# Kernel optimization log

Measured on AMD Instinct MI355X. Metric: run time of the kernel, lower is better.

The kernel has to match this reference:

```python
import jax, jax.numpy as jnp
import numpy as np

K = 256       # num states
M = 2         # markov order
D = 256       # lemb_size
V = 50000     # ntypes (vocab)
T = 512
B = 256
Kp1 = K + 1
EPS = 1e-5
INIT = 0.1


def _layernorm(h, g, b):
    mu = h.mean(-1, keepdims=True)
    var = ((h - mu) ** 2).mean(-1, keepdims=True)
    return (h - mu) / jnp.sqrt(var + EPS) * g + b


def setup_inputs() -> dict:
    key = jax.random.key(0)
    ks = jax.random.split(key, 12)
    u = lambda k, shp: jax.random.uniform(k, shp, jnp.float32, -INIT, INIT)
    return {
        "x": jax.random.randint(ks[0], (T, B), 0, V, dtype=jnp.int32),
        "z": jax.random.randint(ks[1], (T, B), 0, K, dtype=jnp.int32),
        "lembs": u(ks[2], (K, D)),
        "tlembs": u(ks[3], (Kp1, D)),
        "dec_W": u(ks[4], (V, D)),
        "dec_b": jnp.zeros((V,), jnp.float32),
        "em_W": u(ks[5], (D, D)),
        "em_bias": jnp.zeros((D,), jnp.float32),
        "em_g": jnp.ones((D,), jnp.float32),
        "em_beta": jnp.zeros((D,), jnp.float32),
        "td_W": u(ks[6], (K, M * D)),
        "td_b": jnp.zeros((K,), jnp.float32),
        "tm_W": u(ks[7], (M * D, M * D)),
        "tm_bias": jnp.zeros((M * D,), jnp.float32),
        "tn_g": jnp.ones((M * D,), jnp.float32),
        "tn_beta": jnp.zeros((M * D,), jnp.float32),
    }


def reference(x, z, lembs, tlembs, dec_W, dec_b, em_W, em_bias, em_g, em_beta,
              td_W, td_b, tm_W, tm_bias, tn_g, tn_beta):
    # --- emission distribution: K x V log-normalized ---
    h = _layernorm(lembs + jax.nn.relu(lembs @ em_W.T + em_bias), em_g, em_beta)
    emdist = jax.nn.log_softmax(h @ dec_W.T + dec_b, axis=1)  # (K, V)

    # --- transition distribution: (Kp1^M, K) log-normalized ---
    # cartesian product of label embeddings, row-major: row r <-> (i_0,...,i_{M-1})
    idx = jnp.indices((Kp1,) * M).reshape(M, -1)                 # (M, Kp1^M)
    cat = tlembs[idx].transpose(1, 0, 2).reshape(-1, M * D)      # (Kp1^M, M*D)
    th = _layernorm(cat + jax.nn.relu(cat @ tm_W.T + tm_bias), tn_g, tn_beta)
    transdist = jax.nn.log_softmax(th @ td_W.T + td_b, axis=1)   # (Kp1^M, K)

    # --- log_joint ---
    xlps = emdist.T[x]                                           # (T, B, K)
    emlps = jnp.take_along_axis(xlps, z[..., None].astype(jnp.int32), axis=2)[..., 0].sum(0)  # (B,)

    zpad = jnp.concatenate([jnp.full((M, B), K, dtype=z.dtype), z], axis=0)  # (T+M, B)
    win = jnp.stack([zpad[m:m + T] for m in range(M + 1)], 0)    # (M+1, T, B)
    lin = win[0]
    for m in range(1, M):
        lin = lin * Kp1 + win[m]                                 # row index into (Kp1^M, K)
    trans_lps = transdist[lin, win[M]]                           # (T, B)
    return emlps + trans_lps.sum(0)                              # (B,)
```

## Files before the change

### kernel.cpp

```cpp
#include <hip/hip_runtime.h>

#define Kst 256
#define Dd 256
#define Vv 50000
#define VPAD 50176
#define Tt 512
#define Bb 256
#define KP1 257
#define MD 512
#define NROWS (KP1*KP1)
#define EPSf 1e-5f

#define VB2 196
#define NP1 (VB2*4)
#define NTR ((NROWS+31)/32)
#define EMB 800

typedef __attribute__((ext_vector_type(8))) short short8;
typedef __attribute__((ext_vector_type(4))) float f32x4;
typedef __attribute__((ext_vector_type(4))) unsigned u32x4;
typedef __attribute__((ext_vector_type(2))) unsigned u32x2;

__device__ __forceinline__ unsigned short f2bf(float f) {
    unsigned u = __builtin_bit_cast(unsigned, f);
    unsigned r = (u + 0x7fffu + ((u >> 16) & 1u)) >> 16;
    return (unsigned short)r;
}
__device__ __forceinline__ float bf2f(unsigned short u) {
    return __builtin_bit_cast(float, ((unsigned)u) << 16);
}
__device__ __forceinline__ unsigned bfpack(float lo, float hi) {
    return __builtin_amdgcn_perm(__builtin_bit_cast(unsigned, hi),
                                 __builtin_bit_cast(unsigned, lo), 0x07060302u);
}
__device__ __forceinline__ unsigned f2bf2(float lo, float hi) {
    return (unsigned)f2bf(lo) | ((unsigned)f2bf(hi) << 16);
}

union HPU {
    struct { short ta[32][264]; float lsep[4][32][2]; float musig[32][2]; } g;
    struct { short pl[64][266]; } p;
};

__global__ __launch_bounds__(256) void k_hP(
    const float* __restrict__ lembs, const float* __restrict__ em_W,
    const float* __restrict__ em_bias, const float* __restrict__ em_g,
    const float* __restrict__ em_beta, unsigned short* __restrict__ h_bf,
    const float* __restrict__ tlembs, const float* __restrict__ tm_W,
    float* __restrict__ P0, float* __restrict__ P1,
    const float* __restrict__ td_W, const float* __restrict__ tn_g,
    const float* __restrict__ tn_beta, const float* __restrict__ td_b,
    unsigned short* __restrict__ tdwg_bf, float* __restrict__ Gt,
    float* __restrict__ Bt, const float* __restrict__ dec_W,
    unsigned short* __restrict__ dwP)
{
    __shared__ HPU su;
    int bid = blockIdx.x;
    int tid = threadIdx.x, lane = tid & 63, wv = tid >> 6;
    int l15 = lane & 15, q = lane >> 4;

    if (bid >= 108) {
        int pb = bid - 108;
        int vb2 = pb >> 2, c = pb & 3;
        short (*pl)[266] = su.p.pl;
        int base_row = vb2*256 + c*64;
        #pragma unroll 4
        for (int i = 0; i < 16; ++i) {
            int row = wv*16 + i;
            int grow = base_row + row; if (grow > Vv-1) grow = Vv-1;
            float4 f = ((const float4*)(dec_W + (size_t)grow*Dd))[lane];
            u32x2 w; w.x = bfpack(f.x, f.y); w.y = bfpack(f.z, f.w);
            *(u32x2*)&pl[row][lane*4] = w;
        }
        __syncthreads();
        #pragma unroll
        for (int i = 0; i < 8; ++i) {
            short8 val = *(const short8*)&pl[(lane & 15)*4 + wv][i*32 + (lane >> 4)*8];
            *(short8*)(dwP + ((size_t)vb2*8192 + (size_t)i*1024
                              + (c*4 + wv)*64 + lane)*8) = val;
        }
        return;
    }

    if (bid >= 44) {
        int c = (bid - 44)*4 + wv;
        const float4* w4 = (const float4*)(td_W + (size_t)c*MD);
        const float4* g4 = (const float4*)tn_g;
        const float4* b4 = (const float4*)tn_beta;
        float sg = 0.f, sb = 0.f;
        short8 o;
        #pragma unroll
        for (int u = 0; u < 2; ++u) {
            int j4 = lane*2 + u;
            float4 w = w4[j4], g = g4[j4], bt = b4[j4];
            sg += w.x*g.x + w.y*g.y + w.z*g.z + w.w*g.w;
            sb += w.x*bt.x + w.y*bt.y + w.z*bt.z + w.w*bt.w;
            o[u*4+0] = (short)f2bf(w.x*g.x);
            o[u*4+1] = (short)f2bf(w.y*g.y);
            o[u*4+2] = (short)f2bf(w.z*g.z);
            o[u*4+3] = (short)f2bf(w.w*g.w);
        }
        {
            int wvv = c >> 6, l15v = (c >> 2) & 15, ctv = c & 3;
            int ksv = lane >> 2, qv = lane & 3;
            *(short8*)(tdwg_bf +
                ((((size_t)wvv*16 + ksv)*4 + ctv)*64 + (qv*16 + l15v))*8) = o;
        }
        #pragma unroll
        for (int dd = 32; dd > 0; dd >>= 1) {
            sg += __shfl_xor(sg, dd);
            sb += __shfl_xor(sb, dd);
        }
        if (lane == 0) { Gt[c] = sg; Bt[c] = sb + td_b[c]; }
        return;
    }

    short (*ta)[264] = su.g.ta;
    float (*lsep)[32][2] = su.g.lsep;
    float (*musig)[2] = su.g.musig;

    int job, r0, cb, koff, BK;
    const float* Arow; const float* Brow;
    if (bid < 8) {
        job = 0; r0 = bid*32; cb = 0; koff = 0; BK = Dd;
        Arow = lembs; Brow = em_W;
    } else {
        int b2 = bid - 8;
        int half = b2 / 18;
        int b3 = b2 % 18;
        job = 1 + half;
        r0 = (b3 >> 1) * 32;
        cb = (b3 & 1) * 256;
        koff = half * 256; BK = MD;
        Arow = tlembs; Brow = tm_W;
    }

    {
        int row = tid >> 3, seg = (tid & 7) * 32;
        int r = r0 + row;
        if (r > 256) r = 256;
        const float4* s4 = (const float4*)(Arow + (size_t)r*Dd + seg);
        #pragma unroll
        for (int u = 0; u < 4; ++u) {
            float4 f0 = s4[u*2], f1 = s4[u*2+1];
            u32x4 pk;
            pk.x = bfpack(f0.x, f0.y);
            pk.y = bfpack(f0.z, f0.w);
            pk.z = bfpack(f1.x, f1.y);
            pk.w = bfpack(f1.z, f1.w);
            *(short8*)&ta[row][seg + u*8] = __builtin_bit_cast(short8, pk);
        }
    }
    __syncthreads();

    const float* bptr[4];
    #pragma unroll
    for (int ct = 0; ct < 4; ++ct) {
        int j = cb + wv*64 + ct*16 + l15;
        bptr[ct] = Brow + (size_t)j*BK + koff + q*8;
    }
    f32x4 acc[2][4];
    #pragma unroll
    for (int rt = 0; rt < 2; ++rt)
        #pragma unroll
        for (int ct = 0; ct < 4; ++ct)
            acc[rt][ct] = (f32x4){0.f,0.f,0.f,0.f};
    for (int ks = 0; ks < 8; ++ks) {
        short8 a0 = *(const short8*)&ta[ 0 + l15][ks*32 + q*8];
        short8 a1 = *(const short8*)&ta[16 + l15][ks*32 + q*8];
        short8 b[4];
        #pragma unroll
        for (int ct = 0; ct < 4; ++ct) {
            float4 f0 = *(const float4*)(bptr[ct] + ks*32);
            float4 f1 = *(const float4*)(bptr[ct] + ks*32 + 4);
            u32x4 pk;
            pk.x = bfpack(f0.x, f0.y);
            pk.y = bfpack(f0.z, f0.w);
            pk.z = bfpack(f1.x, f1.y);
            pk.w = bfpack(f1.z, f1.w);
            b[ct] = __builtin_bit_cast(short8, pk);
        }
        #pragma unroll
        for (int ct = 0; ct < 4; ++ct) {
            acc[0][ct] = __builtin_amdgcn_mfma_f32_16x16x32_bf16(a0, b[ct], acc[0][ct], 0,0,0);
            acc[1][ct] = __builtin_amdgcn_mfma_f32_16x16x32_bf16(a1, b[ct], acc[1][ct], 0,0,0);
        }
    }

    if (job != 0) {
        float* Pd = (job == 1) ? P0 : P1;
        #pragma unroll
        for (int rt = 0; rt < 2; ++rt) {
            #pragma unroll
            for (int reg = 0; reg < 4; ++reg) {
                int r = r0 + rt*16 + q*4 + reg;
                if (r < KP1) {
                    float* dst = Pd + (size_t)r*MD + cb + wv*64;
                    #pragma unroll
                    for (int ct = 0; ct < 4; ++ct)
                        dst[ct*16 + l15] = acc[rt][ct][reg];
                }
            }
        }
        return;
    }

    float bias_c[4];
    #pragma unroll
    for (int ct = 0; ct < 4; ++ct)
        bias_c[ct] = em_bias[wv*64 + ct*16 + l15];
    #pragma unroll
    for (int rt = 0; rt < 2; ++rt) {
        #pragma unroll
        for (int reg = 0; reg < 4; ++reg) {
            int r = r0 + rt*16 + q*4 + reg;
            #pragma unroll
            for (int ct = 0; ct < 4; ++ct) {
                float lv = lembs[(size_t)r*Dd + wv*64 + ct*16 + l15];
                acc[rt][ct][reg] = lv + fmaxf(acc[rt][ct][reg] + bias_c[ct], 0.f);
            }
        }
    }
    #pragma unroll
    for (int rt = 0; rt < 2; ++rt) {
        #pragma unroll
        for (int reg = 0; reg < 4; ++reg) {
            float s  = ((acc[rt][0][reg] + acc[rt][1][reg]) + (acc[rt][2][reg] + acc[rt][3][reg]));
            float ss = ((acc[rt][0][reg]*acc[rt][0][reg] + acc[rt][1][reg]*acc[rt][1][reg])
                      + (acc[rt][2][reg]*acc[rt][2][reg] + acc[rt][3][reg]*acc[rt][3][reg]));
            s  += __shfl_xor(s, 1);  ss += __shfl_xor(ss, 1);
            s  += __shfl_xor(s, 2);  ss += __shfl_xor(ss, 2);
            s  += __shfl_xor(s, 4);  ss += __shfl_xor(ss, 4);
            s  += __shfl_xor(s, 8);  ss += __shfl_xor(ss, 8);
            if (l15 == 0) {
                int rw = rt*16 + q*4 + reg;
                lsep[wv][rw][0] = s;
                lsep[wv][rw][1] = ss;
            }
        }
    }
    __syncthreads();
    if (tid < 32) {
        float s  = (lsep[0][tid][0] + lsep[1][tid][0]) + (lsep[2][tid][0] + lsep[3][tid][0]);
        float ss = (lsep[0][tid][1] + lsep[1][tid][1]) + (lsep[2][tid][1] + lsep[3][tid][1]);
        float mu = s * (1.f/Dd);
        musig[tid][0] = mu;
        musig[tid][1] = rsqrtf(ss*(1.f/Dd) - mu*mu + EPSf);
    }
    __syncthreads();
    float gl[4], bl[4];
    #pragma unroll
    for (int ct = 0; ct < 4; ++ct) {
        gl[ct] = em_g[wv*64 + ct*16 + l15];
        bl[ct] = em_beta[wv*64 + ct*16 + l15];
    }
    #pragma unroll
    for (int rt = 0; rt < 2; ++rt) {
        #pragma unroll
        for (int reg = 0; reg < 4; ++reg) {
            int rw = rt*16 + q*4 + reg;
            int r = r0 + rw;
            float mu = musig[rw][0], rs = musig[rw][1];
            unsigned short* dst = h_bf + (size_t)r*Dd + wv*64;
            #pragma unroll
            for (int ct = 0; ct < 4; ++ct)
                dst[ct*16 + l15] = f2bf((acc[rt][ct][reg] - mu)*rs*gl[ct] + bl[ct]);
        }
    }
}

union SMemU {
    struct { short hs[64][264]; } em;
    struct { short th[32][520]; float musig[32][2]; float lsep[4][32][2]; } tr;
};

__global__ __launch_bounds__(256, 4) void k_emtrans(
    const unsigned short* __restrict__ dwP, const float* __restrict__ dec_b,
    const unsigned short* __restrict__ h_bf, float* __restrict__ part1,
    unsigned short* __restrict__ E2,
    const float* __restrict__ tlembs, const float* __restrict__ P0,
    const float* __restrict__ P1, const float* __restrict__ tm_bias,
    const short* __restrict__ tdwg_bf, const float* __restrict__ Gt,
    const float* __restrict__ Bt, float* __restrict__ lse_t,
    unsigned short* __restrict__ Td)
{
    __shared__ SMemU sm;
    int bid = blockIdx.x;
    int tid = threadIdx.x, lane = tid & 63, wv = tid >> 6;
    int l15 = lane & 15, q = lane >> 4;

    if (bid < EMB) {
        int xcd = bid & 7, slot = bid >> 3;
        int g2 = slot >> 2, kg = slot & 3;
        int vb = g2*8 + xcd;
        if (vb >= VB2) return;
        short (*hs)[264] = sm.em.hs;

        {
            int row = tid >> 2, c0 = (tid & 3) * 64;
            const short8* src = (const short8*)(h_bf + (size_t)(kg*64 + row)*Dd + c0);
            #pragma unroll
            for (int u = 0; u < 8; ++u)
                *(short8*)&hs[row][c0 + u*8] = src[u];
        }
        __syncthreads();

        f32x4 acc[4][4];
        #pragma unroll
        for (int mt = 0; mt < 4; ++mt)
            #pragma unroll
            for (int ct = 0; ct < 4; ++ct)
                acc[mt][ct] = (f32x4){0.f,0.f,0.f,0.f};

        const short8* bb8 = (const short8*)dwP + ((size_t)vb*8*16 + wv*4)*64 + lane;
        short8 Bf[3][4];
        #define LDB_EM(slot_, kk) { \
            Bf[slot_][0] = bb8[((kk)*16 + 0)*64]; \
            Bf[slot_][1] = bb8[((kk)*16 + 1)*64]; \
            Bf[slot_][2] = bb8[((kk)*16 + 2)*64]; \
            Bf[slot_][3] = bb8[((kk)*16 + 3)*64]; }
        LDB_EM(0, 0)
        LDB_EM(1, 1)
        #pragma unroll
        for (int ks = 0; ks < 8; ++ks) {
            if (ks < 6) LDB_EM((ks+2)%3, ks+2)
            short8 a[4];
            #pragma unroll
            for (int mt = 0; mt < 4; ++mt)
                a[mt] = *(const short8*)&hs[mt*16 + l15][ks*32 + q*8];
            #pragma unroll
            for (int mt = 0; mt < 4; ++mt)
                #pragma unroll
                for (int ct = 0; ct < 4; ++ct)
                    acc[mt][ct] = __builtin_amdgcn_mfma_f32_16x16x32_bf16(a[mt], Bf[ks%3][ct], acc[mt][ct], 0,0,0);
        }
        #undef LDB_EM

        int vcol[4]; bool vok[4];
        #pragma unroll
        for (int ct = 0; ct < 4; ++ct) {
            int v = vb*256 + wv*64 + l15*4 + ct;
            vok[ct] = (v < Vv);
            vcol[ct] = v < Vv ? v : Vv-1;
        }
        #pragma unroll
        for (int ct = 0; ct < 4; ++ct) {
            if (vok[ct]) {
                float db = dec_b[vcol[ct]];
                #pragma unroll
                for (int mt = 0; mt < 4; ++mt)
                    #pragma unroll
                    for (int reg = 0; reg < 4; ++reg)
                        acc[mt][ct][reg] += db;
            } else {
                #pragma unroll
                for (int mt = 0; mt < 4; ++mt)
                    #pragma unroll
                    for (int reg = 0; reg < 4; ++reg)
                        acc[mt][ct][reg] = -1e30f;
            }
        }
        #pragma unroll
        for (int mt = 0; mt < 4; ++mt) {
            #pragma unroll
            for (int reg = 0; reg < 4; ++reg) {
                int k = kg*64 + mt*16 + q*4 + reg;
                u32x2 p;
                p.x = f2bf2(acc[mt][0][reg], acc[mt][1][reg]);
                p.y = f2bf2(acc[mt][2][reg], acc[mt][3][reg]);
                *(u32x2*)(E2 + (size_t)k*VPAD + vb*256 + wv*64 + l15*4) = p;
            }
        }
        #pragma unroll
        for (int mt = 0; mt < 4; ++mt) {
            #pragma unroll
            for (int reg = 0; reg < 4; ++reg) {
                float s = (__expf(acc[mt][0][reg]) + __expf(acc[mt][1][reg]))
                        + (__expf(acc[mt][2][reg]) + __expf(acc[mt][3][reg]));
                s += __shfl_xor(s, 1);
                s += __shfl_xor(s, 2);
                s += __shfl_xor(s, 4);
                s += __shfl_xor(s, 8);
                if (l15 == 0) {
                    int k = kg*64 + mt*16 + q*4 + reg;
                    part1[(size_t)(vb*4 + wv)*256 + k] = s;
                }
            }
        }
        return;
    }

    int tr_id = bid - EMB;
    if (tr_id >= NTR) return;
    short (*th)[520]   = sm.tr.th;
    float (*musig)[2]  = sm.tr.musig;
    float (*lsep)[32][2] = sm.tr.lsep;
    int r0 = tr_id * 32;

    {
        const float4* bias0 = (const float4*)tm_bias;
        const float4* bias1 = (const float4*)(tm_bias + 256);
        float4 c0 = bias0[lane], c1 = bias1[lane];
        int i0a[8], i1a[8];
        #pragma unroll
        for (int i = 0; i < 8; ++i) {
            int r = r0 + wv*8 + i; if (r >= NROWS) r = NROWS - 1;
            i0a[i] = r / KP1; i1a[i] = r - i0a[i]*KP1;
        }
        #define ROWBODY(i, A0, B0, T0, A1, B1, T1) { \
            int row = wv*8 + (i); \
            float v0 = (T0).x + fmaxf((A0).x+(B0).x+c0.x, 0.f); \
            float v1 = (T0).y + fmaxf((A0).y+(B0).y+c0.y, 0.f); \
            float v2 = (T0).z + fmaxf((A0).z+(B0).z+c0.z, 0.f); \
            float v3 = (T0).w + fmaxf((A0).w+(B0).w+c0.w, 0.f); \
            float v4 = (T1).x + fmaxf((A1).x+(B1).x+c1.x, 0.f); \
            float v5 = (T1).y + fmaxf((A1).y+(B1).y+c1.y, 0.f); \
            float v6 = (T1).z + fmaxf((A1).z+(B1).z+c1.z, 0.f); \
            float v7 = (T1).w + fmaxf((A1).w+(B1).w+c1.w, 0.f); \
            u32x2 p0; p0.x = bfpack(v0, v1); p0.y = bfpack(v2, v3); \
            u32x2 p1; p1.x = bfpack(v4, v5); p1.y = bfpack(v6, v7); \
            *(u32x2*)&th[row][lane*4]       = p0; \
            *(u32x2*)&th[row][256 + lane*4] = p1; \
            float s  = ((v0+v1)+(v2+v3)) + ((v4+v5)+(v6+v7)); \
            float ss = ((v0*v0+v1*v1)+(v2*v2+v3*v3)) + ((v4*v4+v5*v5)+(v6*v6+v7*v7)); \
            _Pragma("unroll") \
            for (int d = 1; d < 64; d <<= 1) { \
                s  += __shfl_xor(s, d); \
                ss += __shfl_xor(ss, d); \
            } \
            if (lane == 0) { \
                float mu = s * (1.f/MD); \
                musig[row][0] = mu; \
                musig[row][1] = rsqrtf(ss*(1.f/MD) - mu*mu + EPSf); \
            } }

        if (i0a[0] == i0a[7]) {
            float4 A0 = ((const float4*)(P0 + (size_t)i0a[0]*MD))[lane];
            float4 A1 = ((const float4*)(P0 + (size_t)i0a[0]*MD + 256))[lane];
            float4 T0 = ((const float4*)(tlembs + (size_t)i0a[0]*Dd))[lane];
            float4 b0 = ((const float4*)(P1 + (size_t)i1a[0]*MD))[lane];
            float4 b1 = ((const float4*)(P1 + (size_t)i1a[0]*MD + 256))[lane];
            float4 t1 = ((const float4*)(tlembs + (size_t)i1a[0]*Dd))[lane];
            #pragma unroll
            for (int i = 0; i < 8; ++i) {
                float4 nb0, nb1, nt1;
                if (i < 7) {
                    nb0 = ((const float4*)(P1 + (size_t)i1a[i+1]*MD))[lane];
                    nb1 = ((const float4*)(P1 + (size_t)i1a[i+1]*MD + 256))[lane];
                    nt1 = ((const float4*)(tlembs + (size_t)i1a[i+1]*Dd))[lane];
                }
                ROWBODY(i, A0, b0, T0, A1, b1, t1)
                b0 = nb0; b1 = nb1; t1 = nt1;
            }
        } else {
            float4 A0 = ((const float4*)(P0 + (size_t)i0a[0]*MD))[lane];
            float4 A1 = ((const float4*)(P0 + (size_t)i0a[0]*MD + 256))[lane];
            float4 T0 = ((const float4*)(tlembs + (size_t)i0a[0]*Dd))[lane];
            float4 b0 = ((const float4*)(P1 + (size_t)i1a[0]*MD))[lane];
            float4 b1 = ((const float4*)(P1 + (size_t)i1a[0]*MD + 256))[lane];
            float4 t1 = ((const float4*)(tlembs + (size_t)i1a[0]*Dd))[lane];
            #pragma unroll
            for (int i = 0; i < 8; ++i) {
                float4 nA0, nA1, nT0, nb0, nb1, nt1;
                if (i < 7) {
                    nA0 = ((const float4*)(P0 + (size_t)i0a[i+1]*MD))[lane];
                    nA1 = ((const float4*)(P0 + (size_t)i0a[i+1]*MD + 256))[lane];
                    nT0 = ((const float4*)(tlembs + (size_t)i0a[i+1]*Dd))[lane];
                    nb0 = ((const float4*)(P1 + (size_t)i1a[i+1]*MD))[lane];
                    nb1 = ((const float4*)(P1 + (size_t)i1a[i+1]*MD + 256))[lane];
                    nt1 = ((const float4*)(tlembs + (size_t)i1a[i+1]*Dd))[lane];
                }
                ROWBODY(i, A0, b0, T0, A1, b1, t1)
                A0 = nA0; A1 = nA1; T0 = nT0; b0 = nb0; b1 = nb1; t1 = nt1;
            }
        }
        #undef ROWBODY
    }
    __syncthreads();

    f32x4 acc[2][4];
    #pragma unroll
    for (int rt = 0; rt < 2; ++rt)
        #pragma unroll
        for (int ct = 0; ct < 4; ++ct)
            acc[rt][ct] = (f32x4){0.f, 0.f, 0.f, 0.f};
    const short* bb = tdwg_bf + (size_t)wv*32768 + (size_t)lane*8;
    short8 Bf[3][4];
    #define LDB_TR(slot_, kk) { const short* nxt = bb + (size_t)(kk)*2048; \
        Bf[slot_][0] = *(const short8*)(nxt); \
        Bf[slot_][1] = *(const short8*)(nxt + 512); \
        Bf[slot_][2] = *(const short8*)(nxt + 1024); \
        Bf[slot_][3] = *(const short8*)(nxt + 1536); }
    LDB_TR(0, 0)
    LDB_TR(1, 1)
    #pragma unroll
    for (int ks = 0; ks < 16; ++ks) {
        if (ks < 14) LDB_TR((ks+2)%3, ks+2)
        int ko = ks*32 + q*8;
        short8 a0 = *(const short8*)&th[ 0 + l15][ko];
        short8 a1 = *(const short8*)&th[16 + l15][ko];
        acc[0][0] = __builtin_amdgcn_mfma_f32_16x16x32_bf16(a0, Bf[ks%3][0], acc[0][0], 0,0,0);
        acc[1][0] = __builtin_amdgcn_mfma_f32_16x16x32_bf16(a1, Bf[ks%3][0], acc[1][0], 0,0,0);
        acc[0][1] = __builtin_amdgcn_mfma_f32_16x16x32_bf16(a0, Bf[ks%3][1], acc[0][1], 0,0,0);
        acc[1][1] = __builtin_amdgcn_mfma_f32_16x16x32_bf16(a1, Bf[ks%3][1], acc[1][1], 0,0,0);
        acc[0][2] = __builtin_amdgcn_mfma_f32_16x16x32_bf16(a0, Bf[ks%3][2], acc[0][2], 0,0,0);
        acc[1][2] = __builtin_amdgcn_mfma_f32_16x16x32_bf16(a1, Bf[ks%3][2], acc[1][2], 0,0,0);
        acc[0][3] = __builtin_amdgcn_mfma_f32_16x16x32_bf16(a0, Bf[ks%3][3], acc[0][3], 0,0,0);
        acc[1][3] = __builtin_amdgcn_mfma_f32_16x16x32_bf16(a1, Bf[ks%3][3], acc[1][3], 0,0,0);
    }
    #undef LDB_TR

    float4 Gc = *(const float4*)(Gt + wv*64 + l15*4);
    float4 Bc = *(const float4*)(Bt + wv*64 + l15*4);
    #pragma unroll
    for (int rt = 0; rt < 2; ++rt) {
        #pragma unroll
        for (int reg = 0; reg < 4; ++reg) {
            int rw = rt*16 + q*4 + reg;
            float mu = musig[rw][0], rs = musig[rw][1];
            float e0 = rs*(acc[rt][0][reg] - mu*Gc.x) + Bc.x;
            float e1 = rs*(acc[rt][1][reg] - mu*Gc.y) + Bc.y;
            float e2 = rs*(acc[rt][2][reg] - mu*Gc.z) + Bc.z;
            float e3 = rs*(acc[rt][3][reg] - mu*Gc.w) + Bc.w;
            long r = (long)r0 + rw;
            if (r < NROWS) {
                u32x2 p;
                p.x = f2bf2(e0, e1);
                p.y = f2bf2(e2, e3);
                *(u32x2*)(Td + (size_t)r*Kst + wv*64 + l15*4) = p;
            }
            float m = fmaxf(fmaxf(e0, e1), fmaxf(e2, e3));
            m = fmaxf(m, __shfl_xor(m, 1));
            m = fmaxf(m, __shfl_xor(m, 2));
            m = fmaxf(m, __shfl_xor(m, 4));
            m = fmaxf(m, __shfl_xor(m, 8));
            float s = __expf(e0 - m) + __expf(e1 - m) + __expf(e2 - m) + __expf(e3 - m);
            s += __shfl_xor(s, 1);
            s += __shfl_xor(s, 2);
            s += __shfl_xor(s, 4);
            s += __shfl_xor(s, 8);
            if (l15 == 0) {
                lsep[wv][rw][0] = m;
                lsep[wv][rw][1] = s;
            }
        }
    }
    __syncthreads();
    if (tid < 32) {
        int r = r0 + tid;
        if (r < NROWS) {
            float m0 = lsep[0][tid][0], m1 = lsep[1][tid][0];
            float m2 = lsep[2][tid][0], m3 = lsep[3][tid][0];
            float mg = fmaxf(fmaxf(m0, m1), fmaxf(m2, m3));
            float s = lsep[0][tid][1]*__expf(m0-mg) + lsep[1][tid][1]*__expf(m1-mg)
                    + lsep[2][tid][1]*__expf(m2-mg) + lsep[3][tid][1]*__expf(m3-mg);
            lse_t[r] = mg + logf(s);
        }
    }
}

__global__ __launch_bounds__(256) void k_lse8(
    const float* __restrict__ part1, float* __restrict__ lpart)
{
    __shared__ float lemp[4][256];
    int tid = threadIdx.x, lane = tid & 63, w = tid >> 6;
    const f32x4* p4 = (const f32x4*)part1;
    f32x4 s4 = (f32x4){0.f,0.f,0.f,0.f};
    int j0 = blockIdx.x * 98;
    for (int j = j0 + w; j < j0 + 98; j += 4) {
        f32x4 v = p4[(size_t)j*64 + lane];
        s4.x += v.x; s4.y += v.y; s4.z += v.z; s4.w += v.w;
    }
    *(f32x4*)&lemp[w][lane*4] = s4;
    __syncthreads();
    lpart[blockIdx.x*256 + tid] = (lemp[0][tid] + lemp[1][tid]) + (lemp[2][tid] + lemp[3][tid]);
}

__global__ __launch_bounds__(256) void k_gather7(
    const int* __restrict__ x, const int* __restrict__ z,
    const unsigned short* __restrict__ E2, const float* __restrict__ lpart,
    const unsigned short* __restrict__ Td, const float* __restrict__ lse_t,
    float* __restrict__ gpart)
{
    __shared__ float lem[256];
    int tid = threadIdx.x;
    {
        float s = 0.f;
        #pragma unroll
        for (int r = 0; r < 8; ++r) s += lpart[r*256 + tid];
        lem[tid] = logf(s);
    }
    __syncthreads();

    int b = tid;
    int t0 = blockIdx.x * 8;
    int zm1 = (t0 >= 1) ? z[(t0-1)*Bb + b] : Kst;
    int zm2 = (t0 >= 2) ? z[(t0-2)*Bb + b] : Kst;
    float accv = 0.f;
    #pragma unroll
    for (int u = 0; u < 8; ++u) {
        int t = t0 + u;
        int zc = z[t*Bb + b];
        int xv = x[t*Bb + b];
        int lin = zm2*KP1 + zm1;
        accv += bf2f(E2[(size_t)zc*VPAD + xv]) - lem[zc]
              + bf2f(Td[(size_t)lin*Kst + zc]) - lse_t[lin];
        zm2 = zm1; zm1 = zc;
    }
    gpart[blockIdx.x*Bb + b] = accv;
}

__global__ __launch_bounds__(256) void k_fin(
    const float* __restrict__ gpart, float* __restrict__ out)
{
    int b = threadIdx.x;
    float s = 0.f;
    #pragma unroll 8
    for (int r = 0; r < 64; ++r)
        s += gpart[r*Bb + b];
    out[b] = s;
}

extern "C" void kernel_launch(void* const* d_in, const int* in_sizes, int n_in,
                              void* d_out, int out_size, void* d_ws, size_t ws_size,
                              hipStream_t stream)
{
    const int*   x       = (const int*)  d_in[0];
    const int*   z       = (const int*)  d_in[1];
    const float* lembs   = (const float*)d_in[2];
    const float* tlembs  = (const float*)d_in[3];
    const float* dec_W   = (const float*)d_in[4];
    const float* dec_b   = (const float*)d_in[5];
    const float* em_W    = (const float*)d_in[6];
    const float* em_bias = (const float*)d_in[7];
    const float* em_g    = (const float*)d_in[8];
    const float* em_beta = (const float*)d_in[9];
    const float* td_W    = (const float*)d_in[10];
    const float* td_b    = (const float*)d_in[11];
    const float* tm_W    = (const float*)d_in[12];
    const float* tm_bias = (const float*)d_in[13];
    const float* tn_g    = (const float*)d_in[14];
    const float* tn_beta = (const float*)d_in[15];
    float* out = (float*)d_out;

    float* ws     = (float*)d_ws;
    float* P0     = ws;
    float* P1     = P0 + 131584;
    float* part1  = P1 + 131584;
    float* lpart  = part1 + 200704;
    float* gpart  = lpart + 2048;
    float* lse_t  = gpart + 16384;
    float* Gt     = lse_t + 66052;
    float* Bt     = Gt + 256;
    unsigned short* tdwg_bf = (unsigned short*)(Bt + 256);
    unsigned short* h_bf   = tdwg_bf + 131072;
    unsigned short* E2     = h_bf + 65536;
    unsigned short* Td     = E2 + (size_t)Kst*VPAD;
    unsigned short* dwP    = Td + (size_t)NROWS*Kst;

    k_hP<<<108 + 784, 256, 0, stream>>>(lembs, em_W, em_bias, em_g, em_beta, h_bf,
                                        tlembs, tm_W, P0, P1,
                                        td_W, tn_g, tn_beta, td_b, tdwg_bf, Gt, Bt,
                                        dec_W, dwP);
    k_emtrans<<<EMB + NTR, 256, 0, stream>>>(
        dwP, dec_b, h_bf, part1, E2,
        tlembs, P0, P1, tm_bias, (const short*)tdwg_bf, Gt, Bt, lse_t, Td);
    k_lse8<<<8, 256, 0, stream>>>(part1, lpart);
    k_gather7<<<64, 256, 0, stream>>>(x, z, E2, lpart, Td, lse_t, gpart);
    k_fin<<<1, 256, 0, stream>>>(gpart, out);
}
```

Baseline: 203.6 us.

## Split weight packing into separate kernel and prepack em_W/tm_W into MFMA layout

Moves em_W and tm_W bf16 conversion into a new packing kernel that writes them in MFMA fragment order, so the small GEMM kernel loads ready-made bf16 fragments instead of converting fp32 on the fly. The epilogues now use a permuted column mapping so each lane writes float4/packed stores and reads vectorized bias, gamma and beta. The software-prefetch double buffering in the transition row loop is removed in favour of direct loads. The cost is an extra kernel launch with a serial dependency, and the row loop may lose latency hiding.

Result: slower. 210.9 us (+3.6%).

```diff
diff --git a/kernel.cpp b/kernel.cpp
--- a/kernel.cpp
+++ b/kernel.cpp
@@ -37,32 +37,21 @@
     return (unsigned)f2bf(lo) | ((unsigned)f2bf(hi) << 16);
 }
 
-union HPU {
-    struct { short ta[32][264]; float lsep[4][32][2]; float musig[32][2]; } g;
-    struct { short pl[64][266]; } p;
-};
-
-__global__ __launch_bounds__(256) void k_hP(
-    const float* __restrict__ lembs, const float* __restrict__ em_W,
-    const float* __restrict__ em_bias, const float* __restrict__ em_g,
-    const float* __restrict__ em_beta, unsigned short* __restrict__ h_bf,
-    const float* __restrict__ tlembs, const float* __restrict__ tm_W,
-    float* __restrict__ P0, float* __restrict__ P1,
+__global__ __launch_bounds__(256) void k_pack(
+    const float* __restrict__ dec_W, unsigned short* __restrict__ dwP,
+    const float* __restrict__ em_W, unsigned short* __restrict__ emWP,
+    const float* __restrict__ tm_W, unsigned short* __restrict__ tmWP,
     const float* __restrict__ td_W, const float* __restrict__ tn_g,
     const float* __restrict__ tn_beta, const float* __restrict__ td_b,
     unsigned short* __restrict__ tdwg_bf, float* __restrict__ Gt,
-    float* __restrict__ Bt, const float* __restrict__ dec_W,
-    unsigned short* __restrict__ dwP)
+    float* __restrict__ Bt)
 {
-    __shared__ HPU su;
+    __shared__ short pl[64][266];
     int bid = blockIdx.x;
     int tid = threadIdx.x, lane = tid & 63, wv = tid >> 6;
-    int l15 = lane & 15, q = lane >> 4;
-
-    if (bid >= 108) {
-        int pb = bid - 108;
-        int vb2 = pb >> 2, c = pb & 3;
-        short (*pl)[266] = su.p.pl;
+
+    if (bid < 784) {
+        int vb2 = bid >> 2, c = bid & 3;
         int base_row = vb2*256 + c*64;
         #pragma unroll 4
         for (int i = 0; i < 16; ++i) {
@@ -81,9 +70,46 @@
         }
         return;
     }
-
-    if (bid >= 44) {
-        int c = (bid - 44)*4 + wv;
+    if (bid < 788) {
+        int jc = bid - 784;
+        #pragma unroll 4
+        for (int i = 0; i < 16; ++i) {
+            int row = wv*16 + i;
+            int j = jc*64 + row;
+            float4 f = ((const float4*)(em_W + (size_t)j*Dd))[lane];
+            u32x2 w; w.x = bfpack(f.x, f.y); w.y = bfpack(f.z, f.w);
+            *(u32x2*)&pl[row][lane*4] = w;
+        }
+        __syncthreads();
+        #pragma unroll
+        for (int i = 0; i < 8; ++i) {
+            short8 val = *(const short8*)&pl[(lane & 15)*4 + wv][i*32 + (lane >> 4)*8];
+            *(short8*)(emWP + ((size_t)(i*16 + jc*4 + wv)*64 + lane)*8) = val;
+        }
+        return;
+    }
+    if (bid < 804) {
+        int idx = bid - 788;
+        int jb = idx >> 3, t = idx & 7, jc = t >> 1, kh = t & 1;
+        #pragma unroll 4
+        for (int i = 0; i < 16; ++i) {
+            int row = wv*16 + i;
+            int j = jb*256 + jc*64 + row;
+            float4 f = ((const float4*)(tm_W + (size_t)j*MD + kh*256))[lane];
+            u32x2 w; w.x = bfpack(f.x, f.y); w.y = bfpack(f.z, f.w);
+            *(u32x2*)&pl[row][lane*4] = w;
+        }
+        __syncthreads();
+        #pragma unroll
+        for (int i = 0; i < 8; ++i) {
+            int ksG = kh*8 + i;
+            short8 val = *(const short8*)&pl[(lane & 15)*4 + wv][i*32 + (lane >> 4)*8];
+            *(short8*)(tmWP + ((size_t)((jb*16 + ksG)*16 + jc*4 + wv)*64 + lane)*8) = val;
+        }
+        return;
+    }
+    {
+        int c = (bid - 804)*4 + wv;
         const float4* w4 = (const float4*)(td_W + (size_t)c*MD);
         const float4* g4 = (const float4*)tn_g;
         const float4* b4 = (const float4*)tn_beta;
@@ -112,18 +138,30 @@
             sb += __shfl_xor(sb, dd);
         }
         if (lane == 0) { Gt[c] = sg; Bt[c] = sb + td_b[c]; }
-        return;
-    }
-
-    short (*ta)[264] = su.g.ta;
-    float (*lsep)[32][2] = su.g.lsep;
-    float (*musig)[2] = su.g.musig;
-
-    int job, r0, cb, koff, BK;
-    const float* Arow; const float* Brow;
+    }
+}
+
+__global__ __launch_bounds__(256) void k_hP2(
+    const float* __restrict__ lembs, const float* __restrict__ em_bias,
+    const float* __restrict__ em_g, const float* __restrict__ em_beta,
+    unsigned short* __restrict__ h_bf, const float* __restrict__ tlembs,
+    float* __restrict__ P0, float* __restrict__ P1,
+    const unsigned short* __restrict__ emWP, const unsigned short* __restrict__ tmWP)
+{
+    __shared__ short ta[32][264];
+    __shared__ float lsep[4][32][2];
+    __shared__ float musig[32][2];
+    int bid = blockIdx.x;
+    int tid = threadIdx.x, lane = tid & 63, wv = tid >> 6;
+    int l15 = lane & 15, q = lane >> 4;
+
+    int job, r0, cb;
+    const float* Arow;
+    const short8* bb8;
     if (bid < 8) {
-        job = 0; r0 = bid*32; cb = 0; koff = 0; BK = Dd;
-        Arow = lembs; Brow = em_W;
+        job = 0; r0 = bid*32; cb = 0;
+        Arow = lembs;
+        bb8 = (const short8*)emWP + (size_t)(wv*4)*64 + lane;
     } else {
         int b2 = bid - 8;
         int half = b2 / 18;
@@ -131,8 +169,9 @@
         job = 1 + half;
         r0 = (b3 >> 1) * 32;
         cb = (b3 & 1) * 256;
-        koff = half * 256; BK = MD;
-        Arow = tlembs; Brow = tm_W;
+        int jb = cb >> 8;
+        Arow = tlembs;
+        bb8 = (const short8*)tmWP + ((size_t)(jb*16 + half*8)*16 + wv*4)*64 + lane;
     }
 
     {
@@ -153,38 +192,28 @@
     }
     __syncthreads();
 
-    const float* bptr[4];
-    #pragma unroll
-    for (int ct = 0; ct < 4; ++ct) {
-        int j = cb + wv*64 + ct*16 + l15;
-        bptr[ct] = Brow + (size_t)j*BK + koff + q*8;
-    }
     f32x4 acc[2][4];
     #pragma unroll
     for (int rt = 0; rt < 2; ++rt)
         #pragma unroll
         for (int ct = 0; ct < 4; ++ct)
             acc[rt][ct] = (f32x4){0.f,0.f,0.f,0.f};
+    #pragma unroll
     for (int ks = 0; ks < 8; ++ks) {
         short8 a0 = *(const short8*)&ta[ 0 + l15][ks*32 + q*8];
         short8 a1 = *(const short8*)&ta[16 + l15][ks*32 + q*8];
-        short8 b[4];
-        #pragma unroll
-        for (int ct = 0; ct < 4; ++ct) {
-            float4 f0 = *(const float4*)(bptr[ct] + ks*32);
-            float4 f1 = *(const float4*)(bptr[ct] + ks*32 + 4);
-            u32x4 pk;
-            pk.x = bfpack(f0.x, f0.y);
-            pk.y = bfpack(f0.z, f0.w);
-            pk.z = bfpack(f1.x, f1.y);
-            pk.w = bfpack(f1.z, f1.w);
-            b[ct] = __builtin_bit_cast(short8, pk);
-        }
-        #pragma unroll
-        for (int ct = 0; ct < 4; ++ct) {
-            acc[0][ct] = __builtin_amdgcn_mfma_f32_16x16x32_bf16(a0, b[ct], acc[0][ct], 0,0,0);
-            acc[1][ct] = __builtin_amdgcn_mfma_f32_16x16x32_bf16(a1, b[ct], acc[1][ct], 0,0,0);
-        }
+        short8 b0 = bb8[(ks*16 + 0)*64];
+        short8 b1 = bb8[(ks*16 + 1)*64];
+        short8 b2 = bb8[(ks*16 + 2)*64];
+        short8 b3 = bb8[(ks*16 + 3)*64];
+        acc[0][0] = __builtin_amdgcn_mfma_f32_16x16x32_bf16(a0, b0, acc[0][0], 0,0,0);
+        acc[1][0] = __builtin_amdgcn_mfma_f32_16x16x32_bf16(a1, b0, acc[1][0], 0,0,0);
+        acc[0][1] = __builtin_amdgcn_mfma_f32_16x16x32_bf16(a0, b1, acc[0][1], 0,0,0);
+        acc[1][1] = __builtin_amdgcn_mfma_f32_16x16x32_bf16(a1, b1, acc[1][1], 0,0,0);
+        acc[0][2] = __builtin_amdgcn_mfma_f32_16x16x32_bf16(a0, b2, acc[0][2], 0,0,0);
+        acc[1][2] = __builtin_amdgcn_mfma_f32_16x16x32_bf16(a1, b2, acc[1][2], 0,0,0);
+        acc[0][3] = __builtin_amdgcn_mfma_f32_16x16x32_bf16(a0, b3, acc[0][3], 0,0,0);
+        acc[1][3] = __builtin_amdgcn_mfma_f32_16x16x32_bf16(a1, b3, acc[1][3], 0,0,0);
     }
 
     if (job != 0) {
@@ -195,30 +224,27 @@
             for (int reg = 0; reg < 4; ++reg) {
                 int r = r0 + rt*16 + q*4 + reg;
                 if (r < KP1) {
-                    float* dst = Pd + (size_t)r*MD + cb + wv*64;
-                    #pragma unroll
-                    for (int ct = 0; ct < 4; ++ct)
-                        dst[ct*16 + l15] = acc[rt][ct][reg];
+                    float4 o;
+                    o.x = acc[rt][0][reg]; o.y = acc[rt][1][reg];
+                    o.z = acc[rt][2][reg]; o.w = acc[rt][3][reg];
+                    *(float4*)(Pd + (size_t)r*MD + cb + wv*64 + l15*4) = o;
                 }
             }
         }
         return;
     }
 
-    float bias_c[4];
-    #pragma unroll
-    for (int ct = 0; ct < 4; ++ct)
-        bias_c[ct] = em_bias[wv*64 + ct*16 + l15];
+    float4 bias4 = *(const float4*)(em_bias + wv*64 + l15*4);
     #pragma unroll
     for (int rt = 0; rt < 2; ++rt) {
         #pragma unroll
         for (int reg = 0; reg < 4; ++reg) {
             int r = r0 + rt*16 + q*4 + reg;
-            #pragma unroll
-            for (int ct = 0; ct < 4; ++ct) {
-                float lv = lembs[(size_t)r*Dd + wv*64 + ct*16 + l15];
-                acc[rt][ct][reg] = lv + fmaxf(acc[rt][ct][reg] + bias_c[ct], 0.f);
-            }
+            float4 lv = *(const float4*)(lembs + (size_t)r*Dd + wv*64 + l15*4);
+            acc[rt][0][reg] = lv.x + fmaxf(acc[rt][0][reg] + bias4.x, 0.f);
+            acc[rt][1][reg] = lv.y + fmaxf(acc[rt][1][reg] + bias4.y, 0.f);
+            acc[rt][2][reg] = lv.z + fmaxf(acc[rt][2][reg] + bias4.z, 0.f);
+            acc[rt][3][reg] = lv.w + fmaxf(acc[rt][3][reg] + bias4.w, 0.f);
         }
     }
     #pragma unroll
@@ -248,12 +274,8 @@
         musig[tid][1] = rsqrtf(ss*(1.f/Dd) - mu*mu + EPSf);
     }
     __syncthreads();
-    float gl[4], bl[4];
-    #pragma unroll
-    for (int ct = 0; ct < 4; ++ct) {
-        gl[ct] = em_g[wv*64 + ct*16 + l15];
-        bl[ct] = em_beta[wv*64 + ct*16 + l15];
-    }
+    float4 g4  = *(const float4*)(em_g + wv*64 + l15*4);
+    float4 be4 = *(const float4*)(em_beta + wv*64 + l15*4);
     #pragma unroll
     for (int rt = 0; rt < 2; ++rt) {
         #pragma unroll
@@ -261,10 +283,14 @@
             int rw = rt*16 + q*4 + reg;
             int r = r0 + rw;
             float mu = musig[rw][0], rs = musig[rw][1];
-            unsigned short* dst = h_bf + (size_t)r*Dd + wv*64;
-            #pragma unroll
-            for (int ct = 0; ct < 4; ++ct)
-                dst[ct*16 + l15] = f2bf((acc[rt][ct][reg] - mu)*rs*gl[ct] + bl[ct]);
+            float e0 = (acc[rt][0][reg] - mu)*rs*g4.x + be4.x;
+            float e1 = (acc[rt][1][reg] - mu)*rs*g4.y + be4.y;
+            float e2 = (acc[rt][2][reg] - mu)*rs*g4.z + be4.z;
+            float e3 = (acc[rt][3][reg] - mu)*rs*g4.w + be4.w;
+            u32x2 p;
+            p.x = f2bf2(e0, e1);
+            p.y = f2bf2(e2, e3);
+            *(u32x2*)(h_bf + (size_t)r*Dd + wv*64 + l15*4) = p;
         }
     }
 }
@@ -438,40 +464,23 @@
             float4 A0 = ((const float4*)(P0 + (size_t)i0a[0]*MD))[lane];
             float4 A1 = ((const float4*)(P0 + (size_t)i0a[0]*MD + 256))[lane];
             float4 T0 = ((const float4*)(tlembs + (size_t)i0a[0]*Dd))[lane];
-            float4 b0 = ((const float4*)(P1 + (size_t)i1a[0]*MD))[lane];
-            float4 b1 = ((const float4*)(P1 + (size_t)i1a[0]*MD + 256))[lane];
-            float4 t1 = ((const float4*)(tlembs + (size_t)i1a[0]*Dd))[lane];
             #pragma unroll
             for (int i = 0; i < 8; ++i) {
-                float4 nb0, nb1, nt1;
-                if (i < 7) {
-                    nb0 = ((const float4*)(P1 + (size_t)i1a[i+1]*MD))[lane];
-                    nb1 = ((const float4*)(P1 + (size_t)i1a[i+1]*MD + 256))[lane];
-                    nt1 = ((const float4*)(tlembs + (size_t)i1a[i+1]*Dd))[lane];
-                }
+                float4 b0 = ((const float4*)(P1 + (size_t)i1a[i]*MD))[lane];
+                float4 b1 = ((const float4*)(P1 + (size_t)i1a[i]*MD + 256))[lane];
+                float4 t1 = ((const float4*)(tlembs + (size_t)i1a[i]*Dd))[lane];
                 ROWBODY(i, A0, b0, T0, A1, b1, t1)
-                b0 = nb0; b1 = nb1; t1 = nt1;
             }
         } else {
-            float4 A0 = ((const float4*)(P0 + (size_t)i0a[0]*MD))[lane];
-            float4 A1 = ((const float4*)(P0 + (size_t)i0a[0]*MD + 256))[lane];
-            float4 T0 = ((const float4*)(tlembs + (size_t)i0a[0]*Dd))[lane];
-            float4 b0 = ((const float4*)(P1 + (size_t)i1a[0]*MD))[lane];
-            float4 b1 = ((const float4*)(P1 + (size_t)i1a[0]*MD + 256))[lane];
-            float4 t1 = ((const float4*)(tlembs + (size_t)i1a[0]*Dd))[lane];
             #pragma unroll
             for (int i = 0; i < 8; ++i) {
-                float4 nA0, nA1, nT0, nb0, nb1, nt1;
-                if (i < 7) {
-                    nA0 = ((const float4*)(P0 + (size_t)i0a[i+1]*MD))[lane];
-                    nA1 = ((const float4*)(P0 + (size_t)i0a[i+1]*MD + 256))[lane];
-                    nT0 = ((const float4*)(tlembs + (size_t)i0a[i+1]*Dd))[lane];
-                    nb0 = ((const float4*)(P1 + (size_t)i1a[i+1]*MD))[lane];
-                    nb1 = ((const float4*)(P1 + (size_t)i1a[i+1]*MD + 256))[lane];
-                    nt1 = ((const float4*)(tlembs + (size_t)i1a[i+1]*Dd))[lane];
-                }
+                float4 A0 = ((const float4*)(P0 + (size_t)i0a[i]*MD))[lane];
+                float4 A1 = ((const float4*)(P0 + (size_t)i0a[i]*MD + 256))[lane];
+                float4 T0 = ((const float4*)(tlembs + (size_t)i0a[i]*Dd))[lane];
+                float4 b0 = ((const float4*)(P1 + (size_t)i1a[i]*MD))[lane];
+                float4 b1 = ((const float4*)(P1 + (size_t)i1a[i]*MD + 256))[lane];
+                float4 t1 = ((const float4*)(tlembs + (size_t)i1a[i]*Dd))[lane];
                 ROWBODY(i, A0, b0, T0, A1, b1, t1)
-                A0 = nA0; A1 = nA1; T0 = nT0; b0 = nb0; b1 = nb1; t1 = nt1;
             }
         }
         #undef ROWBODY
@@ -657,11 +666,13 @@
     unsigned short* E2     = h_bf + 65536;
     unsigned short* Td     = E2 + (size_t)Kst*VPAD;
     unsigned short* dwP    = Td + (size_t)NROWS*Kst;
-
-    k_hP<<<108 + 784, 256, 0, stream>>>(lembs, em_W, em_bias, em_g, em_beta, h_bf,
-                                        tlembs, tm_W, P0, P1,
-                                        td_W, tn_g, tn_beta, td_b, tdwg_bf, Gt, Bt,
-                                        dec_W, dwP);
+    unsigned short* emWP   = dwP + (size_t)VPAD*Kst;
+    unsigned short* tmWP   = emWP + 65536;
+
+    k_pack<<<868, 256, 0, stream>>>(dec_W, dwP, em_W, emWP, tm_W, tmWP,
+                                    td_W, tn_g, tn_beta, td_b, tdwg_bf, Gt, Bt);
+    k_hP2<<<44, 256, 0, stream>>>(lembs, em_bias, em_g, em_beta, h_bf,
+                                  tlembs, P0, P1, emWP, tmWP);
     k_emtrans<<<EMB + NTR, 256, 0, stream>>>(
         dwP, dec_b, h_bf, part1, E2,
         tlembs, P0, P1, tm_bias, (const short*)tdwg_bf, Gt, Bt, lse_t, Td);
```
